# Performance work log

Hardware: AMD Instinct MI355X
Metric: run time of the kernel (lower is better)

The kernel has to match this reference:

```python
import jax, jax.numpy as jnp
import numpy as np

D_MODEL = 512
N_HEADS = 8
HEAD_DIM = D_MODEL // N_HEADS
MAX_LAG = 10
NEG_INF = -1e9


def setup_inputs() -> dict:
    key = jax.random.key(0)
    ks = jax.random.split(key, 10)
    B, S, D = 4, 2048, D_MODEL
    x = jax.random.normal(ks[0], (B, S, D), dtype=jnp.float32)
    w = lambda k: jax.random.normal(k, (D, D), dtype=jnp.float32) * 0.02
    b = lambda k: jax.random.normal(k, (D,), dtype=jnp.float32) * 0.02
    return {
        "x": x,
        "Wq": w(ks[1]), "bq": b(ks[2]),
        "Wk": w(ks[3]), "bk": b(ks[4]),
        "Wv": w(ks[5]), "bv": b(ks[6]),
        "Wo": w(ks[7]), "bo": b(ks[8]),
        "temporal_decay": jnp.ones((MAX_LAG + 1,), dtype=jnp.float32),
    }


def _temporal_bias(seq_len, temporal_decay):
    # decay[lag] = -log(softplus(p[lag]) + 1e-8) for lag <= MAX_LAG, else NEG_INF
    d = -jnp.log(jax.nn.softplus(temporal_decay) + 1e-8)  # [MAX_LAG+1]
    i = jnp.arange(seq_len)
    lag = jnp.abs(i[:, None] - i[None, :])  # [S,S]
    return jnp.where(lag <= MAX_LAG, d[jnp.clip(lag, 0, MAX_LAG)], NEG_INF)


def reference(x, Wq, bq, Wk, bk, Wv, bv, Wo, bo, temporal_decay):
    B, S, D = x.shape
    H, hd = N_HEADS, HEAD_DIM
    q = (x @ Wq + bq).reshape(B, S, H, hd)
    k = (x @ Wk + bk).reshape(B, S, H, hd)
    v = (x @ Wv + bv).reshape(B, S, H, hd)
    scale = jnp.sqrt(jnp.float32(hd))
    scores = jnp.einsum("bihd,bjhd->bhij", q, k) / scale  # [B,H,S,S]
    bias = _temporal_bias(S, temporal_decay)  # [S,S]
    scores = scores + bias[None, None]
    causal = jnp.tril(jnp.ones((S, S), dtype=bool))
    scores = jnp.where(causal[None, None], scores, NEG_INF)  # masked_fill
    attn = jax.nn.softmax(scores, axis=-1)  # dropout is identity at eval
    ctx = jnp.einsum("bhij,bjhd->bihd", attn, v).reshape(B, S, D)
    out = ctx @ Wo + bo
    return out, attn.mean(axis=1)
```

## Files before the change

kernel.cpp:

```cpp
#include <hip/hip_runtime.h>
#include <hip/hip_bf16.h>
#include <math.h>

constexpr int Bsz = 4;
constexpr int SEQ = 2048;
constexpr int DM  = 512;
constexpr int NH  = 8;
constexpr int HD  = 64;
constexpr int LAG = 10;
constexpr int MROWS = Bsz * SEQ;
constexpr size_t OUT0_ELEMS = (size_t)Bsz * SEQ * DM;
constexpr int NQKV = 3 * DM;
constexpr int ATTN_V4 = Bsz * SEQ * SEQ / 4;

typedef __attribute__((ext_vector_type(8))) short short8;
typedef __attribute__((ext_vector_type(4))) float f32x4;
typedef __attribute__((ext_vector_type(16))) float f32x16;

__device__ __forceinline__ float bf2f(unsigned short u) {
  union { unsigned int i; float f; } x; x.i = (unsigned int)u << 16; return x.f;
}
__device__ __forceinline__ unsigned short f2bf(float f) {
  __hip_bfloat16 h = __float2bfloat16(f);
  return *(unsigned short*)&h;
}

__device__ __forceinline__ void gload_lds16(const void* g, void* l) {
  __builtin_amdgcn_global_load_lds(
      (const __attribute__((address_space(1))) unsigned int*)g,
      (__attribute__((address_space(3))) unsigned int*)l, 16, 0, 0);
}

__global__ __launch_bounds__(256) void prep(
    const float* __restrict__ x, const float* __restrict__ Wq,
    const float* __restrict__ Wk, const float* __restrict__ Wv,
    const float* __restrict__ Wo, const float* __restrict__ bq,
    const float* __restrict__ bk, const float* __restrict__ bv,
    __hip_bfloat16* __restrict__ xb, __hip_bfloat16* __restrict__ Wtqkv,
    __hip_bfloat16* __restrict__ Wot, float* __restrict__ bcat) {
  __shared__ float t[32][33];
  const int blk = blockIdx.x;
  const int tid = threadIdx.x;
  if (blk < 2048) {
    size_t i = ((size_t)blk * 256 + tid) * 8;
    float4 a = *(const float4*)(x + i);
    float4 b = *(const float4*)(x + i + 4);
    union { unsigned short h[8]; uint4 u; } pk;
    pk.h[0] = f2bf(a.x); pk.h[1] = f2bf(a.y); pk.h[2] = f2bf(a.z); pk.h[3] = f2bf(a.w);
    pk.h[4] = f2bf(b.x); pk.h[5] = f2bf(b.y); pk.h[6] = f2bf(b.z); pk.h[7] = f2bf(b.w);
    *(uint4*)(xb + i) = pk.u;
  } else if (blk < 3072) {
    const int zb = blk - 2048;
    const int z = zb >> 8, rem = zb & 255;
    const float* W = (z == 0) ? Wq : (z == 1) ? Wk : (z == 2) ? Wv : Wo;
    __hip_bfloat16* dst = (z < 3) ? (Wtqkv + (size_t)z * DM * DM) : Wot;
    const int n0 = (rem & 15) * 32, k0 = (rem >> 4) * 32;
    const int tx = tid & 31, ty = tid >> 5;
#pragma unroll
    for (int r = 0; r < 4; r++)
      t[ty + r * 8][tx] = W[(size_t)(k0 + ty + r * 8) * DM + n0 + tx];
    __syncthreads();
#pragma unroll
    for (int r = 0; r < 4; r++)
      dst[(size_t)(n0 + ty + r * 8) * DM + k0 + tx] =
          __float2bfloat16(t[tx][ty + r * 8]);
  } else {
    for (int i = tid; i < NQKV; i += 256)
      bcat[i] = (i < 512) ? bq[i] : (i < 1024) ? bk[i - 512] : bv[i - 1024];
  }
}

__global__ __launch_bounds__(512) void qkv_gemm(
    const __hip_bfloat16* __restrict__ A, const __hip_bfloat16* __restrict__ Bt,
    const float* __restrict__ bias, __hip_bfloat16* __restrict__ C,
    float* __restrict__ fill) {
  __shared__ __align__(16) char smem[114688];

  int lin = blockIdx.x;
  lin = (lin & 7) * 32 + (lin >> 3);
  const int bm = (lin >> 3) * 256;
  const int bn = (lin & 7) * 192;

  const int tid = threadIdx.x;
  const int lane = tid & 63, wave = tid >> 6;
  const int wr = wave >> 1, wc = wave & 1;
  const int l31 = lane & 31, lhi = lane >> 5;
  const int gtid = blockIdx.x * 512 + tid;
  constexpr int GSTRIDE = 256 * 512;

  f32x16 acc[2][3] = {};

  auto STAGE = [&](int buf, int k0) {
    char* base = smem + buf * 57344;
#pragma unroll
    for (int it = 0; it < 4; ++it) {
      const int g = it * 512 + tid;
      const int row = g >> 3, ch = g & 7;
      const int src_ch = ch ^ (row & 7);
      gload_lds16(A + (size_t)(bm + row) * DM + k0 + src_ch * 8,
                  base + (it * 512 + wave * 64) * 16);
    }
    char* baseB = base + 32768;
#pragma unroll
    for (int it = 0; it < 3; ++it) {
      const int g = it * 512 + tid;
      const int row = g >> 3, ch = g & 7;
      const int src_ch = ch ^ (row & 7);
      gload_lds16(Bt + (size_t)(bn + row) * DM + k0 + src_ch * 8,
                  baseB + (it * 512 + wave * 64) * 16);
    }
  };

  STAGE(0, 0);

  for (int t = 0; t < 8; ++t) {
    __syncthreads();
    if (t < 7) STAGE((t + 1) & 1, (t + 1) * 64);

    {
      f32x4 z = {0.f, 0.f, 0.f, 0.f};
#pragma unroll
      for (int j = 0; j < 4; ++j)
        __builtin_nontemporal_store(z, (f32x4*)fill + gtid + (t * 4 + j) * GSTRIDE);
    }

    const char* As = smem + (t & 1) * 57344;
    const char* Bs = As + 32768;
#pragma unroll
    for (int kk = 0; kk < 4; ++kk) {
      short8 a[2], b[3];
#pragma unroll
      for (int fi = 0; fi < 2; ++fi) {
        const int row = wr * 64 + fi * 32 + l31;
        const int ch = (kk * 2 + lhi) ^ (row & 7);
        a[fi] = *(const short8*)(As + row * 128 + ch * 16);
      }
#pragma unroll
      for (int fj = 0; fj < 3; ++fj) {
        const int row = wc * 96 + fj * 32 + l31;
        const int ch = (kk * 2 + lhi) ^ (row & 7);
        b[fj] = *(const short8*)(Bs + row * 128 + ch * 16);
      }
#pragma unroll
      for (int fi = 0; fi < 2; ++fi)
#pragma unroll
        for (int fj = 0; fj < 3; ++fj)
          acc[fi][fj] = __builtin_amdgcn_mfma_f32_32x32x16_bf16(
              a[fi], b[fj], acc[fi][fj], 0, 0, 0);
    }
  }

  __syncthreads();
  unsigned short (*Cs)[192] = (unsigned short (*)[192])smem;
#pragma unroll
  for (int fj = 0; fj < 3; ++fj) {
    const int col = wc * 96 + fj * 32 + l31;
    const float bv = bias[bn + col];
#pragma unroll
    for (int fi = 0; fi < 2; ++fi)
#pragma unroll
      for (int r = 0; r < 16; ++r) {
        const int row = wr * 64 + fi * 32 + (r & 3) + 8 * (r >> 2) + 4 * lhi;
        Cs[row][col] = f2bf(acc[fi][fj][r] + bv);
      }
  }
  __syncthreads();
#pragma unroll
  for (int it = 0; it < 12; ++it) {
    const int g = it * 512 + tid;
    const int row = g / 24, ch = g % 24;
    *(uint4*)(C + (size_t)(bm + row) * NQKV + bn + ch * 8) =
        *(const uint4*)&Cs[row][ch * 8];
  }
}

template <bool OUT_BF16>
__global__ __launch_bounds__(256) void gemm_mfma(
    const __hip_bfloat16* __restrict__ A, const __hip_bfloat16* __restrict__ Bt,
    const float* __restrict__ bias, void* __restrict__ Cout,
    int N, int K, int gx, float* __restrict__ fill) {
  __shared__ __align__(16) char smem[32768];
  unsigned short (*As)[64] = (unsigned short (*)[64])smem;
  unsigned short (*Bs)[64] = (unsigned short (*)[64])(smem + 16384);

  int lin = blockIdx.x;
  const int cpx = gridDim.x >> 3;
  lin = (lin & 7) * cpx + (lin >> 3);
  const int bm = (lin / gx) * 128;
  const int bn = (lin % gx) * 128;

  const int tid = threadIdx.x;
  const int lane = tid & 63, wave = tid >> 6;
  const int wr = wave >> 1, wc = wave & 1;
  const int l31 = lane & 31, lhi = lane >> 5;
  const int gtid = blockIdx.x * 256 + tid;
  const int gstride = gridDim.x << 8;

  f32x16 acc[2][2] = {};

  for (int k0 = 0; k0 < K; k0 += 64) {
#pragma unroll
    for (int it = 0; it < 4; ++it) {
      const int g = it * 256 + tid;
      const int row = g >> 3, ch = g & 7;
      const int src_ch = ch ^ (row & 7);
      gload_lds16(A + (size_t)(bm + row) * K + k0 + src_ch * 8,
                  (char*)As + (it * 256 + wave * 64) * 16);
    }
#pragma unroll
    for (int it = 0; it < 4; ++it) {
      const int g = it * 256 + tid;
      const int row = g >> 3, ch = g & 7;
      const int src_ch = ch ^ (row & 7);
      gload_lds16(Bt + (size_t)(bn + row) * K + k0 + src_ch * 8,
                  (char*)Bs + (it * 256 + wave * 64) * 16);
    }
    __syncthreads();

    if (fill != nullptr) {
      const int step = k0 >> 6;
      f32x4 z = {0.f, 0.f, 0.f, 0.f};
#pragma unroll
      for (int j = 0; j < 3; ++j) {
        const int idx = gtid + (step * 3 + j) * gstride;
        if (idx < ATTN_V4)
          __builtin_nontemporal_store(z, (f32x4*)fill + idx);
      }
    }

#pragma unroll
    for (int kk = 0; kk < 4; ++kk) {
      short8 a[2], b[2];
#pragma unroll
      for (int fi = 0; fi < 2; ++fi) {
        const int row = wr * 64 + fi * 32 + l31;
        const int ch = (kk * 2 + lhi) ^ (row & 7);
        a[fi] = *(const short8*)((const char*)As + row * 128 + ch * 16);
      }
#pragma unroll
      for (int fj = 0; fj < 2; ++fj) {
        const int row = wc * 64 + fj * 32 + l31;
        const int ch = (kk * 2 + lhi) ^ (row & 7);
        b[fj] = *(const short8*)((const char*)Bs + row * 128 + ch * 16);
      }
#pragma unroll
      for (int fi = 0; fi < 2; ++fi)
#pragma unroll
        for (int fj = 0; fj < 2; ++fj)
          acc[fi][fj] = __builtin_amdgcn_mfma_f32_32x32x16_bf16(
              a[fi], b[fj], acc[fi][fj], 0, 0, 0);
    }
    __syncthreads();
  }

  if (OUT_BF16) {
    unsigned short (*Cs)[128] = (unsigned short (*)[128])smem;
#pragma unroll
    for (int fj = 0; fj < 2; ++fj) {
      const float bv = bias[bn + wc * 64 + fj * 32 + l31];
      const int col = wc * 64 + fj * 32 + l31;
#pragma unroll
      for (int fi = 0; fi < 2; ++fi)
#pragma unroll
        for (int r = 0; r < 16; ++r) {
          const int row = wr * 64 + fi * 32 + (r & 3) + 8 * (r >> 2) + 4 * lhi;
          Cs[row][col] = f2bf(acc[fi][fj][r] + bv);
        }
    }
    __syncthreads();
    __hip_bfloat16* C = (__hip_bfloat16*)Cout;
#pragma unroll
    for (int t = 0; t < 8; ++t) {
      const int g = t * 256 + tid;
      const int row = g >> 4, ch = g & 15;
      *(uint4*)(C + (size_t)(bm + row) * N + bn + ch * 8) =
          *(const uint4*)&Cs[row][ch * 8];
    }
  } else {
    float (*Cs)[128] = (float (*)[128])smem;
    float* C = (float*)Cout;
#pragma unroll
    for (int half = 0; half < 2; ++half) {
      if (wr == half) {
#pragma unroll
        for (int fj = 0; fj < 2; ++fj) {
          const float bv = bias[bn + wc * 64 + fj * 32 + l31];
          const int col = wc * 64 + fj * 32 + l31;
#pragma unroll
          for (int fi = 0; fi < 2; ++fi)
#pragma unroll
            for (int r = 0; r < 16; ++r) {
              const int row = fi * 32 + (r & 3) + 8 * (r >> 2) + 4 * lhi;
              Cs[row][col] = acc[fi][fj][r] + bv;
            }
        }
      }
      __syncthreads();
#pragma unroll
      for (int t = 0; t < 8; ++t) {
        const int g = t * 256 + tid;
        const int row = g >> 5, ch = g & 31;
        *(float4*)(C + (size_t)(bm + half * 64 + row) * N + bn + ch * 4) =
            *(const float4*)&Cs[row][ch * 4];
      }
      __syncthreads();
    }
  }
}

__global__ __launch_bounds__(256) void band_attn(
    const __hip_bfloat16* __restrict__ qkv, const float* __restrict__ decay_p,
    __hip_bfloat16* __restrict__ ctx, float* __restrict__ attn_out) {
  __shared__ float dlds[LAG + 1];
  const int tid = threadIdx.x;
  if (tid <= LAG) {
    float p = decay_p[tid];
    float sp = fmaxf(p, 0.0f) + log1pf(expf(-fabsf(p)));
    dlds[tid] = -logf(sp + 1e-8f);
  }
  __syncthreads();

  const int blk = blockIdx.x;
  const int wave = tid >> 6, lane = tid & 63;
  const int bi = ((blk & 7) << 10) + ((blk >> 3) << 2) + wave;
  const int b = bi >> 11;
  const int i = bi & (SEQ - 1);
  const int jlo = (i >= LAG) ? (i - LAG) : 0;
  const int nj = i - jlo + 1;

  const uint4 qu = *(const uint4*)(
      (const unsigned short*)(qkv + (size_t)bi * NQKV) + lane * 8);
  const unsigned short* qp = (const unsigned short*)&qu;
  float qf[8];
#pragma unroll
  for (int e = 0; e < 8; ++e) qf[e] = bf2f(qp[e]);

  float s[LAG + 1];
#pragma unroll
  for (int jj = 0; jj <= LAG; ++jj) {
    const int j = jlo + jj;
    const bool ok = (j <= i);
    const int jc = ok ? j : i;
    const uint4 ku = *(const uint4*)(
        (const unsigned short*)(qkv + ((size_t)b * SEQ + jc) * NQKV + DM) + lane * 8);
    const unsigned short* kp = (const unsigned short*)&ku;
    float part = 0.0f;
#pragma unroll
    for (int e = 0; e < 8; ++e) part += qf[e] * bf2f(kp[e]);
    part += __shfl_xor(part, 1);
    part += __shfl_xor(part, 2);
    part += __shfl_xor(part, 4);
    s[jj] = ok ? (part * 0.125f + dlds[i - j]) : -1e30f;
  }

  float mx = -1e30f;
#pragma unroll
  for (int jj = 0; jj <= LAG; ++jj) mx = fmaxf(mx, s[jj]);
  float sum = 0.0f;
#pragma unroll
  for (int jj = 0; jj <= LAG; ++jj) { s[jj] = expf(s[jj] - mx); sum += s[jj]; }
  const float inv = 1.0f / sum;

  float c[8] = {};
#pragma unroll
  for (int jj = 0; jj <= LAG; ++jj) {
    const float p = s[jj] * inv;
    s[jj] = p;
    const int j = jlo + jj;
    const int jc = (j <= i) ? j : i;
    const uint4 vu = *(const uint4*)(
        (const unsigned short*)(qkv + ((size_t)b * SEQ + jc) * NQKV + 2 * DM) + lane * 8);
    const unsigned short* vp = (const unsigned short*)&vu;
#pragma unroll
    for (int e = 0; e < 8; ++e) c[e] += p * bf2f(vp[e]);
  }

  unsigned short co[8];
#pragma unroll
  for (int e = 0; e < 8; ++e) co[e] = f2bf(c[e]);
  *(uint4*)((unsigned short*)(ctx + (size_t)bi * DM) + lane * 8) = *(const uint4*)co;

#pragma unroll
  for (int jj = 0; jj <= LAG; ++jj) {
    float a = s[jj];
    a += __shfl_xor(a, 8);
    a += __shfl_xor(a, 16);
    a += __shfl_xor(a, 32);
    if (lane == jj && jj < nj)
      __builtin_nontemporal_store(a * 0.125f,
                                  attn_out + (size_t)bi * SEQ + jlo + jj);
  }
}

extern "C" void kernel_launch(void* const* d_in, const int* in_sizes, int n_in,
                              void* d_out, int out_size, void* d_ws, size_t ws_size,
                              hipStream_t stream) {
  const float* x   = (const float*)d_in[0];
  const float* Wq  = (const float*)d_in[1];
  const float* bq  = (const float*)d_in[2];
  const float* Wk  = (const float*)d_in[3];
  const float* bk  = (const float*)d_in[4];
  const float* Wv  = (const float*)d_in[5];
  const float* bv  = (const float*)d_in[6];
  const float* Wo  = (const float*)d_in[7];
  const float* bo  = (const float*)d_in[8];
  const float* dec = (const float*)d_in[9];

  float* out      = (float*)d_out;
  float* attn_out = out + OUT0_ELEMS;

  char* w = (char*)d_ws;
  __hip_bfloat16* xb    = (__hip_bfloat16*)w;  w += (size_t)MROWS * DM * 2;
  __hip_bfloat16* Wtqkv = (__hip_bfloat16*)w;  w += (size_t)NQKV * DM * 2;
  __hip_bfloat16* Wot   = (__hip_bfloat16*)w;  w += (size_t)DM * DM * 2;
  float*          bcat  = (float*)w;           w += (size_t)NQKV * 4;
  __hip_bfloat16* qkv   = (__hip_bfloat16*)w;  w += (size_t)MROWS * NQKV * 2;
  __hip_bfloat16* ctxb  = (__hip_bfloat16*)w;

  prep<<<3073, 256, 0, stream>>>(x, Wq, Wk, Wv, Wo, bq, bk, bv,
                                 xb, Wtqkv, Wot, bcat);

  qkv_gemm<<<256, 512, 0, stream>>>(xb, Wtqkv, bcat, qkv, attn_out);

  band_attn<<<2048, 256, 0, stream>>>(qkv, dec, ctxb, attn_out);

  gemm_mfma<false><<<256, 256, 0, stream>>>(ctxb, Wot, bo, out,
                                            DM, DM, DM / 128, nullptr);
}
```

Measured before the change: 67.64 us.

## Move attention-output zero fill from QKV GEMM into banded attention kernel

```diff
diff --git a/kernel.cpp b/kernel.cpp
--- a/kernel.cpp
+++ b/kernel.cpp
@@ -11,7 +11,6 @@
 constexpr int MROWS = Bsz * SEQ;
 constexpr size_t OUT0_ELEMS = (size_t)Bsz * SEQ * DM;
 constexpr int NQKV = 3 * DM;
-constexpr int ATTN_V4 = Bsz * SEQ * SEQ / 4;
 
 typedef __attribute__((ext_vector_type(8))) short short8;
 typedef __attribute__((ext_vector_type(4))) float f32x4;
@@ -72,8 +71,7 @@
 
 __global__ __launch_bounds__(512) void qkv_gemm(
     const __hip_bfloat16* __restrict__ A, const __hip_bfloat16* __restrict__ Bt,
-    const float* __restrict__ bias, __hip_bfloat16* __restrict__ C,
-    float* __restrict__ fill) {
+    const float* __restrict__ bias, __hip_bfloat16* __restrict__ C) {
   __shared__ __align__(16) char smem[114688];
 
   int lin = blockIdx.x;
@@ -85,8 +83,6 @@
   const int lane = tid & 63, wave = tid >> 6;
   const int wr = wave >> 1, wc = wave & 1;
   const int l31 = lane & 31, lhi = lane >> 5;
-  const int gtid = blockIdx.x * 512 + tid;
-  constexpr int GSTRIDE = 256 * 512;
 
   f32x16 acc[2][3] = {};
 
@@ -117,13 +113,6 @@
     __syncthreads();
     if (t < 7) STAGE((t + 1) & 1, (t + 1) * 64);
 
-    {
-      f32x4 z = {0.f, 0.f, 0.f, 0.f};
-#pragma unroll
-      for (int j = 0; j < 4; ++j)
-        __builtin_nontemporal_store(z, (f32x4*)fill + gtid + (t * 4 + j) * GSTRIDE);
-    }
-
     const char* As = smem + (t & 1) * 57344;
     const char* Bs = As + 32768;
 #pragma unroll
@@ -178,7 +167,7 @@
 __global__ __launch_bounds__(256) void gemm_mfma(
     const __hip_bfloat16* __restrict__ A, const __hip_bfloat16* __restrict__ Bt,
     const float* __restrict__ bias, void* __restrict__ Cout,
-    int N, int K, int gx, float* __restrict__ fill) {
+    int N, int K, int gx) {
   __shared__ __align__(16) char smem[32768];
   unsigned short (*As)[64] = (unsigned short (*)[64])smem;
   unsigned short (*Bs)[64] = (unsigned short (*)[64])(smem + 16384);
@@ -193,8 +182,6 @@
   const int lane = tid & 63, wave = tid >> 6;
   const int wr = wave >> 1, wc = wave & 1;
   const int l31 = lane & 31, lhi = lane >> 5;
-  const int gtid = blockIdx.x * 256 + tid;
-  const int gstride = gridDim.x << 8;
 
   f32x16 acc[2][2] = {};
 
@@ -216,17 +203,6 @@
                   (char*)Bs + (it * 256 + wave * 64) * 16);
     }
     __syncthreads();
-
-    if (fill != nullptr) {
-      const int step = k0 >> 6;
-      f32x4 z = {0.f, 0.f, 0.f, 0.f};
-#pragma unroll
-      for (int j = 0; j < 3; ++j) {
-        const int idx = gtid + (step * 3 + j) * gstride;
-        if (idx < ATTN_V4)
-          __builtin_nontemporal_store(z, (f32x4*)fill + idx);
-      }
-    }
 
 #pragma unroll
     for (int kk = 0; kk < 4; ++kk) {
@@ -328,6 +304,22 @@
   const int jlo = (i >= LAG) ? (i - LAG) : 0;
   const int nj = i - jlo + 1;
 
+  const int lo4 = jlo & ~3;
+  const int hi4 = (i | 3) + 1;
+
+  float* arow = attn_out + (size_t)bi * SEQ;
+
+  {
+    const int c0 = lo4 >> 2, c1 = hi4 >> 2;
+    f32x4 z = {0.f, 0.f, 0.f, 0.f};
+#pragma unroll
+    for (int t = 0; t < 8; ++t) {
+      const int cid = t * 64 + lane;
+      if (cid < c0 || cid >= c1)
+        __builtin_nontemporal_store(z, (f32x4*)arow + cid);
+    }
+  }
+
   const uint4 qu = *(const uint4*)(
       (const unsigned short*)(qkv + (size_t)bi * NQKV) + lane * 8);
   const unsigned short* qp = (const unsigned short*)&qu;
@@ -386,9 +378,17 @@
     a += __shfl_xor(a, 8);
     a += __shfl_xor(a, 16);
     a += __shfl_xor(a, 32);
-    if (lane == jj && jj < nj)
-      __builtin_nontemporal_store(a * 0.125f,
-                                  attn_out + (size_t)bi * SEQ + jlo + jj);
+    s[jj] = a * 0.125f;
+  }
+
+  {
+    float val = 0.0f;
+    const int rel = lo4 + lane - jlo;
+#pragma unroll
+    for (int jj = 0; jj <= LAG; ++jj)
+      val = (rel == jj && jj < nj) ? s[jj] : val;
+    if (lane < hi4 - lo4)
+      __builtin_nontemporal_store(val, arow + lo4 + lane);
   }
 }
 
@@ -420,10 +420,10 @@
   prep<<<3073, 256, 0, stream>>>(x, Wq, Wk, Wv, Wo, bq, bk, bv,
                                  xb, Wtqkv, Wot, bcat);
 
-  qkv_gemm<<<256, 512, 0, stream>>>(xb, Wtqkv, bcat, qkv, attn_out);
+  qkv_gemm<<<256, 512, 0, stream>>>(xb, Wtqkv, bcat, qkv);
 
   band_attn<<<2048, 256, 0, stream>>>(qkv, dec, ctxb, attn_out);
 
   gemm_mfma<false><<<256, 256, 0, stream>>>(ctxb, Wot, bo, out,
-                                            DM, DM, DM / 128, nullptr);
-}
+                                            DM, DM, DM / 128);
+}
```

Measured after the change: 70.07 us. 1.04x slower.
